# Kernel tuning notes

Hardware: AMD Instinct MI355X
Metric: run time of the kernel (lower is better)

The kernel has to match this reference:

```python
import jax, jax.numpy as jnp
import numpy as np

EPS = 1e-5
HEADS, KK, UU, VV, MM = 4, 16, 1, 64, 23
PAD = (MM - 1) // 2


def _bn(x, gamma, beta, mean, var):
    # eval-mode BatchNorm2d over channel axis 1 of (b, c, w, h)
    scale = gamma / jnp.sqrt(var + EPS)
    return (x - mean[:, None, None]) * scale[:, None, None] + beta[:, None, None]


def setup_inputs() -> dict:
    key = jax.random.key(0)
    ks = jax.random.split(key, 13)
    B, C, W, H = 8, 256, 64, 64
    return {
        "x": jax.random.normal(ks[0], (B, C, W, H), jnp.float32),
        "Wq": jax.random.normal(ks[1], (KK * HEADS, C), jnp.float32) * 0.05,
        "q_gamma": jax.random.uniform(ks[2], (KK * HEADS,), jnp.float32),
        "q_beta": jax.random.normal(ks[3], (KK * HEADS,), jnp.float32) * 0.05,
        "q_mean": jax.random.normal(ks[4], (KK * HEADS,), jnp.float32) * 0.05,
        "q_var": jax.random.uniform(ks[5], (KK * HEADS,), jnp.float32) + 0.5,
        "Wk": jax.random.normal(ks[6], (KK * UU, C), jnp.float32) * 0.05,
        "Wv": jax.random.normal(ks[7], (VV * UU, C), jnp.float32) * 0.05,
        "v_gamma": jax.random.uniform(ks[8], (VV * UU,), jnp.float32),
        "v_beta": jax.random.normal(ks[9], (VV * UU,), jnp.float32) * 0.05,
        "v_mean": jax.random.normal(ks[10], (VV * UU,), jnp.float32) * 0.05,
        "v_var": jax.random.uniform(ks[11], (VV * UU,), jnp.float32) + 0.5,
        "embedding": jax.random.normal(ks[12], (KK, UU, 1, MM, MM), jnp.float32),
    }


def reference(x, Wq, q_gamma, q_beta, q_mean, q_var, Wk, Wv, v_gamma, v_beta, v_mean, v_var, embedding):
    b, C, w, h = x.shape
    n = w * h
    # 1x1 conv projections as channel GEMMs
    q = jnp.einsum('bcij,oc->boij', x, Wq)
    q = _bn(q, q_gamma, q_beta, q_mean, q_var).reshape(b, HEADS, KK, n)
    kf = jnp.einsum('bcij,oc->boij', x, Wk).reshape(b, KK, UU, n)
    kf = jax.nn.softmax(kf, axis=-1)  # softmax over spatial positions
    v = jnp.einsum('bcij,oc->boij', x, Wv)
    v = _bn(v, v_gamma, v_beta, v_mean, v_var)  # (b, vv*uu, w, h)
    v_flat = v.reshape(b, VV, UU, n)
    # content lambda
    lambda_c = jnp.einsum('bkum,bvum->bkv', kf, v_flat)
    y_c = jnp.einsum('bhkn,bkv->bhvn', q, lambda_c)
    # positional lambda via depth-1 conv3d over (vv, w, h)
    v5 = v.reshape(b, UU, VV, w, h)
    lambda_p = jax.lax.conv_general_dilated(
        v5, embedding, window_strides=(1, 1, 1),
        padding=[(0, 0), (PAD, PAD), (PAD, PAD)],
        dimension_numbers=('NCDHW', 'OIDHW', 'NCDHW'))  # (b, kk, vv, w, h)
    lambda_p = lambda_p.reshape(b, KK, VV, n)
    y_p = jnp.einsum('bhkn,bkvn->bhvn', q, lambda_p)
    out = (y_c + y_p).reshape(b, HEADS * VV, w, h)
    return out
```

## Files before the change

kernel.cpp:

```cpp
#include <hip/hip_runtime.h>

typedef __attribute__((ext_vector_type(8))) short bf16x8;
typedef __attribute__((ext_vector_type(4))) float f32x4;

#define EPS 1e-5f
#define B 8
#define C 256
#define NPIX 4096
#define NCH 144
#define ROW_V 64
#define ROW_KF 128
#define PAD 11
#define VH_WORDS 3840

#define WP_OFF    0u
#define BIAS_OFF  36864u
#define PROJ_OFF  37120u
#define RMAX_OFF  4755712u
#define LC_OFF    4755968u
#define ET_OFF    4764160u
#define QT_OFF    4811264u
#define OUTT_OFF  6908416u
#define WS_NEED_QT    6908416u
#define WS_NEED_FULL  15297024u

__device__ inline short f2bf(float f) {
  unsigned u = __float_as_uint(f);
  return (short)((u + 0x7fffu + ((u >> 16) & 1u)) >> 16);
}

__global__ __launch_bounds__(256) void k_prep(
    const float* __restrict__ Wq, const float* __restrict__ qg, const float* __restrict__ qb,
    const float* __restrict__ qm, const float* __restrict__ qv,
    const float* __restrict__ Wk, const float* __restrict__ Wv,
    const float* __restrict__ vg, const float* __restrict__ vb,
    const float* __restrict__ vm, const float* __restrict__ vvar,
    const float* __restrict__ emb,
    float* __restrict__ Wt, float* __restrict__ biasp, ushort* __restrict__ etw) {
  int t = threadIdx.x;
  if (blockIdx.x < 144) {
    int o = blockIdx.x;
    const float* src; float s, bias;
    if (o < 64) {
      s = qg[o] * rsqrtf(qv[o] + EPS); bias = qb[o] - qm[o] * s; src = Wq + o * C;
    } else if (o < 128) {
      int i = o - 64;
      s = vg[i] * rsqrtf(vvar[i] + EPS); bias = vb[i] - vm[i] * s; src = Wv + i * C;
    } else {
      int i = o - 128; s = 1.f; bias = 0.f; src = Wk + i * C;
    }
    Wt[t * NCH + o] = src[t] * s;
    if (t == 0) biasp[o] = bias;
  } else {
    int i = (blockIdx.x - 144) * 256 + t;
    int s = i / 11776;
    int r = i % 11776;
    int dy = r / 512;
    int l = (r / 8) % 64;
    int jj = r % 8;
    int f = l & 15, q = l >> 4;
    int dx = q * 8 + jj - s;
    float val = (dx >= 0 && dx < 23) ? emb[f * 529 + dy * 23 + dx] : 0.f;
    unsigned u = __float_as_uint(val);
    etw[i] = (ushort)((u + 0x7fffu + ((u >> 16) & 1u)) >> 16);
  }
}

__global__ __launch_bounds__(256) void k_wprep(
    const float* __restrict__ Wt, ushort* __restrict__ wtA) {
  int i = blockIdx.x * 256 + threadIdx.x;
  int mt = i >> 9;
  int rest = i & 511;
  int kt = rest >> 6;
  int lane = rest & 63;
  int m = mt * 16 + (lane & 15);
  int c0 = kt * 32 + (lane >> 4) * 8;
  ushort* dst = wtA + (size_t)i * 8;
  #pragma unroll
  for (int j = 0; j < 8; j++) {
    float v = Wt[(c0 + j) * NCH + m];
    unsigned u = __float_as_uint(v);
    dst[j] = (ushort)((u + 0x7fffu + ((u >> 16) & 1u)) >> 16);
  }
}

__global__ __launch_bounds__(256) void k_projm(
    const float* __restrict__ x, const ushort* __restrict__ wtA,
    const float* __restrict__ biasp, float* __restrict__ proj) {
  int ntile = blockIdx.x;
  int b = blockIdx.y;
  int t = threadIdx.x;
  int lane = t & 63, w = t >> 6;
  int px = ntile * 64 + w * 16 + (lane & 15);
  int kq = lane >> 4;
  const float* xb = x + (size_t)b * C * NPIX + px;
  const bf16x8* A = (const bf16x8*)wtA;
  f32x4 acc[9];
  #pragma unroll
  for (int i = 0; i < 9; i++) acc[i] = (f32x4)(0.f);
  #pragma unroll 2
  for (int kt = 0; kt < 8; kt++) {
    int c0 = kt * 32 + kq * 8;
    bf16x8 bb;
    #pragma unroll
    for (int j = 0; j < 8; j++) bb[j] = f2bf(xb[(size_t)(c0 + j) * NPIX]);
    #pragma unroll
    for (int mt = 0; mt < 9; mt++) {
      bf16x8 a = A[(mt * 8 + kt) * 64 + lane];
      acc[mt] = __builtin_amdgcn_mfma_f32_16x16x32_bf16(a, bb, acc[mt], 0, 0, 0);
    }
  }
  float* pb = proj + (size_t)b * NCH * NPIX + px;
  #pragma unroll
  for (int mt = 0; mt < 9; mt++) {
    #pragma unroll
    for (int r = 0; r < 4; r++) {
      int ch = mt * 16 + kq * 4 + r;
      pb[(size_t)ch * NPIX] = acc[mt][r] + biasp[ch];
    }
  }
}

__global__ __launch_bounds__(256) void k_proj(
    const float* __restrict__ x, const float* __restrict__ Wt,
    const float* __restrict__ biasp, float* __restrict__ proj) {
  int tile = blockIdx.x;
  int g = blockIdx.y;
  int b = blockIdx.z;
  int t = threadIdx.x;
  int px = tile * 256 + t;
  const float* xb = x + (size_t)b * C * NPIX + px;
  float acc[18];
  #pragma unroll
  for (int i = 0; i < 18; i++) acc[i] = 0.f;
  #pragma unroll 4
  for (int c = 0; c < C; c++) {
    float xv = xb[(size_t)c * NPIX];
    const float* wrow = Wt + c * NCH + g * 18;
    #pragma unroll
    for (int i = 0; i < 18; i++) acc[i] += xv * wrow[i];
  }
  float* ob = proj + ((size_t)b * NCH + g * 18) * NPIX + px;
  #pragma unroll
  for (int i = 0; i < 18; i++) ob[(size_t)i * NPIX] = acc[i] + biasp[g * 18 + i];
}

__global__ __launch_bounds__(256) void k_qtrans(
    const float* __restrict__ proj, float* __restrict__ qT) {
  int ch = blockIdx.x, b = blockIdx.y, t = threadIdx.x;
  __shared__ float buf[4608];
  const float* src = proj + ((size_t)b * NCH + ch) * NPIX;
  for (int it = 0; it < 16; it++) {
    int p = it * 256 + t;
    buf[p + (p >> 3)] = src[p];
  }
  __syncthreads();
  float* dst = qT + ((size_t)b * 64 + ch) * NPIX;
  for (int it = 0; it < 16; it++) {
    int idx = it * 256 + t;
    int s = idx >> 9, i = idx & 511;
    int p = (i >> 3) * 64 + (i & 7) * 8 + s;
    dst[idx] = buf[p + (p >> 3)];
  }
}

__global__ __launch_bounds__(256) void k_vhalo(
    const float* __restrict__ proj, uint* __restrict__ vhg) {
  int v = blockIdx.x, b = blockIdx.y, t = threadIdx.x;
  const float* vrow = proj + ((size_t)b * NCH + ROW_V + v) * NPIX;
  uint* dst = vhg + (size_t)b * NCH * NPIX + (size_t)v * VH_WORDS;
  for (int p2 = t; p2 < 3784; p2 += 256) {
    int hr = p2 / 44;
    int hc = (p2 % 44) * 2;
    int ir = hr - 11;
    int ic0 = hc - 11, ic1 = hc - 10;
    bool rok = (ir >= 0 && ir < 64);
    float f0 = (rok && ic0 >= 0 && ic0 < 64) ? vrow[ir * 64 + ic0] : 0.f;
    float f1 = (rok && ic1 >= 0 && ic1 < 64) ? vrow[ir * 64 + ic1] : 0.f;
    uint u0 = __float_as_uint(f0), u1 = __float_as_uint(f1);
    uint h0 = (u0 + 0x7fffu + ((u0 >> 16) & 1u)) >> 16;
    uint h1 = (u1 + 0x7fffu + ((u1 >> 16) & 1u)) >> 16;
    dst[p2] = (h0 & 0xffffu) | (h1 << 16);
  }
}

__global__ __launch_bounds__(256) void k_lambda_c(
    const float* __restrict__ proj, float* __restrict__ lc, float* __restrict__ S) {
  int split = blockIdx.x;
  int b = blockIdx.y;
  int t = threadIdx.x;
  int lane = t & 63, w = t >> 6;
  int kr = lane & 15;
  int half = lane >> 4;
  const float* kfrow = proj + ((size_t)b * NCH + ROW_KF + kr) * NPIX;
  const float* vrow  = proj + ((size_t)b * NCH + ROW_V + w * 16 + kr) * NPIX;
  f32x4 acc = (f32x4)(0.f);
  float ssum = 0.f;
  #pragma unroll
  for (int c = 0; c < 2; c++) {
    int n0 = split * 64 + c * 32 + half * 8;
    float4 fa0 = *(const float4*)(kfrow + n0);
    float4 fa1 = *(const float4*)(kfrow + n0 + 4);
    float4 fb0 = *(const float4*)(vrow + n0);
    float4 fb1 = *(const float4*)(vrow + n0 + 4);
    float e0 = __expf(fa0.x), e1 = __expf(fa0.y), e2 = __expf(fa0.z), e3 = __expf(fa0.w);
    float e4 = __expf(fa1.x), e5 = __expf(fa1.y), e6 = __expf(fa1.z), e7 = __expf(fa1.w);
    ssum += (e0 + e1 + e2 + e3) + (e4 + e5 + e6 + e7);
    bf16x8 a, bb;
    a[0] = f2bf(e0); a[1] = f2bf(e1); a[2] = f2bf(e2); a[3] = f2bf(e3);
    a[4] = f2bf(e4); a[5] = f2bf(e5); a[6] = f2bf(e6); a[7] = f2bf(e7);
    bb[0] = f2bf(fb0.x); bb[1] = f2bf(fb0.y); bb[2] = f2bf(fb0.z); bb[3] = f2bf(fb0.w);
    bb[4] = f2bf(fb1.x); bb[5] = f2bf(fb1.y); bb[6] = f2bf(fb1.z); bb[7] = f2bf(fb1.w);
    acc = __builtin_amdgcn_mfma_f32_16x16x32_bf16(a, bb, acc, 0, 0, 0);
  }
  #pragma unroll
  for (int r = 0; r < 4; r++) {
    int k = half * 4 + r;
    atomicAdd(&lc[((size_t)b * 16 + k) * 64 + w * 16 + kr], acc[r]);
  }
  if (w == 0) {
    ssum += __shfl_xor(ssum, 16);
    ssum += __shfl_xor(ssum, 32);
    if (lane < 16) atomicAdd(&S[b * 16 + kr], ssum);
  }
}

__global__ __launch_bounds__(256) void k_lcnorm(
    float* __restrict__ lc, const float* __restrict__ S) {
  int i = blockIdx.x * 256 + threadIdx.x;
  lc[i] /= S[i >> 6];
}

__global__ __launch_bounds__(256, 2) void k_conv_mfma(
    const float* __restrict__ proj, const ushort* __restrict__ etw,
    const float* __restrict__ qT, const float* __restrict__ lc,
    const uint* __restrict__ vhg,
    float* __restrict__ outT, float* __restrict__ out, int mode) {
  int s = blockIdx.x;
  int v = blockIdx.y;
  int b = blockIdx.z;
  int t = threadIdx.x;
  __shared__ __align__(16) ushort vh[86 * 88];

  if (mode != 0) {
    const uint4* vsrc = (const uint4*)(vhg + (size_t)b * NCH * NPIX + (size_t)v * VH_WORDS);
    uint4* vdst = (uint4*)vh;
    for (int i = t; i < 946; i += 256) vdst[i] = vsrc[i];
  } else {
    const float* vrow = proj + ((size_t)b * NCH + ROW_V + v) * NPIX;
    for (int i = t; i < 86 * 88; i += 256) {
      int hr = i / 88, hc = i % 88;
      int ir = hr - 11, ic = hc - 11;
      float val = (ir >= 0 && ir < 64 && ic >= 0 && ic < 64) ? vrow[ir * 64 + ic] : 0.f;
      unsigned u = __float_as_uint(val);
      vh[i] = (ushort)((u + 0x7fffu + ((u >> 16) & 1u)) >> 16);
    }
  }
  __syncthreads();

  int lane = t & 63, w = t >> 6;
  int n_ = lane & 15, q = lane >> 4;
  int rn = n_ >> 3, g = n_ & 7;

  f32x4 acc[8];
  #pragma unroll
  for (int i = 0; i < 8; i++) acc[i] = (f32x4)(0.f);

  const bf16x8* vh8 = (const bf16x8*)vh;
  const bf16x8* e8 = (const bf16x8*)etw + (size_t)s * 1472;
  int baseA = (w * 16 + rn) * 11 + g + q;

  bf16x8 bfr[16];
  #pragma unroll
  for (int r = 0; r < 16; r++)
    bfr[(r & 1) * 8 + ((r >> 1) & 7)] = vh8[baseA + r * 11];

  #pragma unroll
  for (int dy = 0; dy < 23; dy++) {
    bf16x8 ef = e8[dy * 64 + lane];
    bf16x8 tmp;
    if (dy + 16 <= 36) tmp = vh8[baseA + (dy + 16) * 11];
    #pragma unroll
    for (int tt = 0; tt < 8; tt++) {
      int r = dy + 2 * tt;
      acc[tt] = __builtin_amdgcn_mfma_f32_16x16x32_bf16(
          ef, bfr[(r & 1) * 8 + ((r >> 1) & 7)], acc[tt], 0, 0, 0);
    }
    if (dy + 16 <= 36) {
      int rr = dy + 16;
      bfr[(rr & 1) * 8 + ((rr >> 1) & 7)] = tmp;
    }
  }

  float lcv[4];
  #pragma unroll
  for (int r = 0; r < 4; r++) lcv[r] = lc[((size_t)b * 16 + q * 4 + r) * 64 + v];

  if (mode != 0) {
    const float* qTb = qT + (size_t)b * 64 * NPIX;
    float* obT = outT + (size_t)b * 256 * NPIX;
    float* ob = out + (size_t)b * 256 * NPIX;
    #pragma unroll
    for (int tt = 0; tt < 8; tt++) {
      int row = w * 16 + 2 * tt + rn;
      int io = s * 512 + row * 8 + g;
      float lam[4];
      #pragma unroll
      for (int r = 0; r < 4; r++) lam[r] = acc[tt][r] + lcv[r];
      float y[4];
      #pragma unroll
      for (int h = 0; h < 4; h++) {
        float a = 0.f;
        #pragma unroll
        for (int r = 0; r < 4; r++)
          a += qTb[(size_t)(h * 16 + q * 4 + r) * NPIX + io] * lam[r];
        y[h] = a;
      }
      #pragma unroll
      for (int h = 0; h < 4; h++) {
        y[h] += __shfl_xor(y[h], 16);
        y[h] += __shfl_xor(y[h], 32);
      }
      if (q == 0) {
        if (mode == 2) {
          #pragma unroll
          for (int h = 0; h < 4; h++) obT[(size_t)(h * 64 + v) * NPIX + io] = y[h];
        } else {
          int p = row * 64 + 8 * g + s;
          #pragma unroll
          for (int h = 0; h < 4; h++) ob[(size_t)(h * 64 + v) * NPIX + p] = y[h];
        }
      }
    }
  } else {
    const float* qbp = proj + (size_t)b * NCH * NPIX;
    float* ob = out + (size_t)b * 256 * NPIX;
    #pragma unroll
    for (int tt = 0; tt < 8; tt++) {
      int p = (w * 16 + 2 * tt + rn) * 64 + 8 * g + s;
      float lam[4];
      #pragma unroll
      for (int r = 0; r < 4; r++) lam[r] = acc[tt][r] + lcv[r];
      float y[4];
      #pragma unroll
      for (int h = 0; h < 4; h++) {
        float a = 0.f;
        #pragma unroll
        for (int r = 0; r < 4; r++)
          a += qbp[(size_t)(h * 16 + q * 4 + r) * NPIX + p] * lam[r];
        y[h] = a;
      }
      #pragma unroll
      for (int h = 0; h < 4; h++) {
        y[h] += __shfl_xor(y[h], 16);
        y[h] += __shfl_xor(y[h], 32);
      }
      if (q == 0) {
        #pragma unroll
        for (int h = 0; h < 4; h++) ob[(size_t)(h * 64 + v) * NPIX + p] = y[h];
      }
    }
  }
}

__global__ __launch_bounds__(256) void k_outtrans(
    const float* __restrict__ outT, float* __restrict__ out) {
  int ch = blockIdx.x, b = blockIdx.y, t = threadIdx.x;
  __shared__ float buf[4608];
  const float* src = outT + ((size_t)b * 256 + ch) * NPIX;
  for (int it = 0; it < 16; it++) {
    int idx = it * 256 + t;
    int s = idx >> 9, i = idx & 511;
    int p = (i >> 3) * 64 + (i & 7) * 8 + s;
    buf[p + (p >> 3)] = src[idx];
  }
  __syncthreads();
  float* dst = out + ((size_t)b * 256 + ch) * NPIX;
  for (int it = 0; it < 16; it++) {
    int p = it * 256 + t;
    dst[p] = buf[p + (p >> 3)];
  }
}

extern "C" void kernel_launch(void* const* d_in, const int* in_sizes, int n_in,
                              void* d_out, int out_size, void* d_ws, size_t ws_size,
                              hipStream_t stream) {
  const float* x    = (const float*)d_in[0];
  const float* Wq   = (const float*)d_in[1];
  const float* qg   = (const float*)d_in[2];
  const float* qbta = (const float*)d_in[3];
  const float* qm   = (const float*)d_in[4];
  const float* qv   = (const float*)d_in[5];
  const float* Wk   = (const float*)d_in[6];
  const float* Wv   = (const float*)d_in[7];
  const float* vg   = (const float*)d_in[8];
  const float* vb   = (const float*)d_in[9];
  const float* vm   = (const float*)d_in[10];
  const float* vvar = (const float*)d_in[11];
  const float* emb  = (const float*)d_in[12];
  float* ws   = (float*)d_ws;
  float* Wt   = ws + WP_OFF;
  float* bp   = ws + BIAS_OFF;
  float* proj = ws + PROJ_OFF;
  float* Sw   = ws + RMAX_OFF;
  float* lcw  = ws + LC_OFF;
  ushort* etw = (ushort*)(ws + ET_OFF);
  float* qT   = ws + QT_OFF;
  float* outT = ws + OUTT_OFF;
  float* out  = (float*)d_out;
  uint* vhg   = (uint*)proj;
  ushort* wtA = (ushort*)qT;

  size_t wsf = ws_size / sizeof(float);
  int mode = (wsf >= WS_NEED_FULL) ? 2 : ((wsf >= WS_NEED_QT) ? 1 : 0);

  hipLaunchKernelGGL(k_prep, dim3(512), dim3(256), 0, stream,
                     Wq, qg, qbta, qm, qv, Wk, Wv, vg, vb, vm, vvar, emb, Wt, bp, etw);
  hipMemsetAsync(Sw, 0, 8448 * sizeof(float), stream);
  if (mode >= 1) {
    hipLaunchKernelGGL(k_wprep, dim3(18), dim3(256), 0, stream, Wt, wtA);
    hipLaunchKernelGGL(k_projm, dim3(64, 8), dim3(256), 0, stream, x, wtA, bp, proj);
    hipLaunchKernelGGL(k_qtrans, dim3(64, 8), dim3(256), 0, stream, proj, qT);
    hipLaunchKernelGGL(k_vhalo, dim3(64, 8), dim3(256), 0, stream, proj, vhg);
  } else {
    hipLaunchKernelGGL(k_proj, dim3(16, 8, 8), dim3(256), 0, stream, x, Wt, bp, proj);
  }
  hipLaunchKernelGGL(k_lambda_c, dim3(64, 8), dim3(256), 0, stream, proj, lcw, Sw);
  hipLaunchKernelGGL(k_lcnorm, dim3(32), dim3(256), 0, stream, lcw, Sw);
  hipLaunchKernelGGL(k_conv_mfma, dim3(8, 64, 8), dim3(256), 0, stream,
                     proj, etw, qT, lcw, vhg, outT, out, mode);
  if (mode == 2)
    hipLaunchKernelGGL(k_outtrans, dim3(256, 8), dim3(256), 0, stream, outT, out);
}
```

Measured before the change: 212.2 us.

## Fuse q transpose and v halo packing into projection epilogue

The projection MFMA kernel now writes the q channels directly in the transposed qT layout and the v channels directly as bf16 into the padded halo buffer, removing the separate k_qtrans and k_vhalo kernels. The weight bf16 packing (k_wprep) and the zeroing of the halo buffer are folded into extra blocks of k_prep, with wtA staged in the output buffer. This cuts launches and a full read and write pass over the q and v planes, at the cost of scattered 2-byte and strided stores and a larger prep grid that zero-fills the halo.

```diff
diff --git a/kernel.cpp b/kernel.cpp
--- a/kernel.cpp
+++ b/kernel.cpp
@@ -36,10 +36,12 @@
     const float* __restrict__ vg, const float* __restrict__ vb,
     const float* __restrict__ vm, const float* __restrict__ vvar,
     const float* __restrict__ emb,
-    float* __restrict__ Wt, float* __restrict__ biasp, ushort* __restrict__ etw) {
+    float* __restrict__ Wt, float* __restrict__ biasp, ushort* __restrict__ etw,
+    ushort* __restrict__ wtA, uint* __restrict__ vhg) {
   int t = threadIdx.x;
-  if (blockIdx.x < 144) {
-    int o = blockIdx.x;
+  int blk = blockIdx.x;
+  if (blk < 144) {
+    int o = blk;
     const float* src; float s, bias;
     if (o < 64) {
       s = qg[o] * rsqrtf(qv[o] + EPS); bias = qb[o] - qm[o] * s; src = Wq + o * C;
@@ -51,8 +53,8 @@
     }
     Wt[t * NCH + o] = src[t] * s;
     if (t == 0) biasp[o] = bias;
-  } else {
-    int i = (blockIdx.x - 144) * 256 + t;
+  } else if (blk < 512) {
+    int i = (blk - 144) * 256 + t;
     int s = i / 11776;
     int r = i % 11776;
     int dy = r / 512;
@@ -61,37 +63,40 @@
     int f = l & 15, q = l >> 4;
     int dx = q * 8 + jj - s;
     float val = (dx >= 0 && dx < 23) ? emb[f * 529 + dy * 23 + dx] : 0.f;
-    unsigned u = __float_as_uint(val);
-    etw[i] = (ushort)((u + 0x7fffu + ((u >> 16) & 1u)) >> 16);
-  }
-}
-
-__global__ __launch_bounds__(256) void k_wprep(
-    const float* __restrict__ Wt, ushort* __restrict__ wtA) {
-  int i = blockIdx.x * 256 + threadIdx.x;
-  int mt = i >> 9;
-  int rest = i & 511;
-  int kt = rest >> 6;
-  int lane = rest & 63;
-  int m = mt * 16 + (lane & 15);
-  int c0 = kt * 32 + (lane >> 4) * 8;
-  ushort* dst = wtA + (size_t)i * 8;
-  #pragma unroll
-  for (int j = 0; j < 8; j++) {
-    float v = Wt[(c0 + j) * NCH + m];
-    unsigned u = __float_as_uint(v);
-    dst[j] = (ushort)((u + 0x7fffu + ((u >> 16) & 1u)) >> 16);
+    etw[i] = (ushort)f2bf(val);
+  } else if (blk < 530) {
+    int i = (blk - 512) * 256 + t;
+    int mt = i >> 9;
+    int rest = i & 511;
+    int kt = rest >> 6;
+    int lane = rest & 63;
+    int m = mt * 16 + (lane & 15);
+    int c0 = kt * 32 + (lane >> 4) * 8;
+    const float* src; float s;
+    if (m < 64) { s = qg[m] * rsqrtf(qv[m] + EPS); src = Wq + m * C; }
+    else if (m < 128) { int ii = m - 64; s = vg[ii] * rsqrtf(vvar[ii] + EPS); src = Wv + ii * C; }
+    else { s = 1.f; src = Wk + (m - 128) * C; }
+    ushort* dst = wtA + (size_t)i * 8;
+    #pragma unroll
+    for (int j = 0; j < 8; j++) dst[j] = (ushort)f2bf(src[c0 + j] * s);
+  } else {
+    int zi = (blk - 530) * 256 + t;
+    int bb = zi / 61440, w4 = zi % 61440;
+    uint4 z; z.x = z.y = z.z = z.w = 0u;
+    ((uint4*)vhg)[(size_t)bb * 147456 + w4] = z;
   }
 }
 
 __global__ __launch_bounds__(256) void k_projm(
     const float* __restrict__ x, const ushort* __restrict__ wtA,
-    const float* __restrict__ biasp, float* __restrict__ proj) {
+    const float* __restrict__ biasp, float* __restrict__ proj,
+    float* __restrict__ qT, uint* __restrict__ vhg) {
   int ntile = blockIdx.x;
   int b = blockIdx.y;
   int t = threadIdx.x;
   int lane = t & 63, w = t >> 6;
-  int px = ntile * 64 + w * 16 + (lane & 15);
+  int col = w * 16 + (lane & 15);
+  int px = ntile * 64 + col;
   int kq = lane >> 4;
   const float* xb = x + (size_t)b * C * NPIX + px;
   const bf16x8* A = (const bf16x8*)wtA;
@@ -110,13 +115,34 @@
       acc[mt] = __builtin_amdgcn_mfma_f32_16x16x32_bf16(a, bb, acc[mt], 0, 0, 0);
     }
   }
+  int idxT = (col & 7) * 512 + ntile * 8 + (col >> 3);
+  float* qTb = qT + (size_t)b * 64 * NPIX;
+  #pragma unroll
+  for (int mt = 0; mt < 4; mt++) {
+    #pragma unroll
+    for (int r = 0; r < 4; r++) {
+      int ch = mt * 16 + kq * 4 + r;
+      qTb[(size_t)ch * NPIX + idxT] = acc[mt][r] + biasp[ch];
+    }
+  }
   float* pb = proj + (size_t)b * NCH * NPIX + px;
   #pragma unroll
-  for (int mt = 0; mt < 9; mt++) {
+  for (int mt = 4; mt < 9; mt++) {
     #pragma unroll
     for (int r = 0; r < 4; r++) {
       int ch = mt * 16 + kq * 4 + r;
       pb[(size_t)ch * NPIX] = acc[mt][r] + biasp[ch];
+    }
+  }
+  ushort* hb = (ushort*)vhg;
+  size_t hbase = (size_t)b * NCH * NPIX * 2 + (size_t)(ntile + 11) * 88 + col + 11;
+  #pragma unroll
+  for (int mt = 4; mt < 8; mt++) {
+    #pragma unroll
+    for (int r = 0; r < 4; r++) {
+      int ch = mt * 16 + kq * 4 + r;
+      int v = ch - 64;
+      hb[hbase + (size_t)v * (VH_WORDS * 2)] = (ushort)f2bf(acc[mt][r] + biasp[ch]);
     }
   }
 }
@@ -143,45 +169,6 @@
   float* ob = proj + ((size_t)b * NCH + g * 18) * NPIX + px;
   #pragma unroll
   for (int i = 0; i < 18; i++) ob[(size_t)i * NPIX] = acc[i] + biasp[g * 18 + i];
-}
-
-__global__ __launch_bounds__(256) void k_qtrans(
-    const float* __restrict__ proj, float* __restrict__ qT) {
-  int ch = blockIdx.x, b = blockIdx.y, t = threadIdx.x;
-  __shared__ float buf[4608];
-  const float* src = proj + ((size_t)b * NCH + ch) * NPIX;
-  for (int it = 0; it < 16; it++) {
-    int p = it * 256 + t;
-    buf[p + (p >> 3)] = src[p];
-  }
-  __syncthreads();
-  float* dst = qT + ((size_t)b * 64 + ch) * NPIX;
-  for (int it = 0; it < 16; it++) {
-    int idx = it * 256 + t;
-    int s = idx >> 9, i = idx & 511;
-    int p = (i >> 3) * 64 + (i & 7) * 8 + s;
-    dst[idx] = buf[p + (p >> 3)];
-  }
-}
-
-__global__ __launch_bounds__(256) void k_vhalo(
-    const float* __restrict__ proj, uint* __restrict__ vhg) {
-  int v = blockIdx.x, b = blockIdx.y, t = threadIdx.x;
-  const float* vrow = proj + ((size_t)b * NCH + ROW_V + v) * NPIX;
-  uint* dst = vhg + (size_t)b * NCH * NPIX + (size_t)v * VH_WORDS;
-  for (int p2 = t; p2 < 3784; p2 += 256) {
-    int hr = p2 / 44;
-    int hc = (p2 % 44) * 2;
-    int ir = hr - 11;
-    int ic0 = hc - 11, ic1 = hc - 10;
-    bool rok = (ir >= 0 && ir < 64);
-    float f0 = (rok && ic0 >= 0 && ic0 < 64) ? vrow[ir * 64 + ic0] : 0.f;
-    float f1 = (rok && ic1 >= 0 && ic1 < 64) ? vrow[ir * 64 + ic1] : 0.f;
-    uint u0 = __float_as_uint(f0), u1 = __float_as_uint(f1);
-    uint h0 = (u0 + 0x7fffu + ((u0 >> 16) & 1u)) >> 16;
-    uint h1 = (u1 + 0x7fffu + ((u1 >> 16) & 1u)) >> 16;
-    dst[p2] = (h0 & 0xffffu) | (h1 << 16);
-  }
 }
 
 __global__ __launch_bounds__(256) void k_lambda_c(
@@ -409,19 +396,18 @@
   float* outT = ws + OUTT_OFF;
   float* out  = (float*)d_out;
   uint* vhg   = (uint*)proj;
-  ushort* wtA = (ushort*)qT;
+  ushort* wtA = (ushort*)out;
 
   size_t wsf = ws_size / sizeof(float);
   int mode = (wsf >= WS_NEED_FULL) ? 2 : ((wsf >= WS_NEED_QT) ? 1 : 0);
 
-  hipLaunchKernelGGL(k_prep, dim3(512), dim3(256), 0, stream,
-                     Wq, qg, qbta, qm, qv, Wk, Wv, vg, vb, vm, vvar, emb, Wt, bp, etw);
+  hipLaunchKernelGGL(k_prep, dim3(mode >= 1 ? 2450 : 512), dim3(256), 0, stream,
+                     Wq, qg, qbta, qm, qv, Wk, Wv, vg, vb, vm, vvar, emb,
+                     Wt, bp, etw, wtA, vhg);
   hipMemsetAsync(Sw, 0, 8448 * sizeof(float), stream);
   if (mode >= 1) {
-    hipLaunchKernelGGL(k_wprep, dim3(18), dim3(256), 0, stream, Wt, wtA);
-    hipLaunchKernelGGL(k_projm, dim3(64, 8), dim3(256), 0, stream, x, wtA, bp, proj);
-    hipLaunchKernelGGL(k_qtrans, dim3(64, 8), dim3(256), 0, stream, proj, qT);
-    hipLaunchKernelGGL(k_vhalo, dim3(64, 8), dim3(256), 0, stream, proj, vhg);
+    hipLaunchKernelGGL(k_projm, dim3(64, 8), dim3(256), 0, stream,
+                       x, wtA, bp, proj, qT, vhg);
   } else {
     hipLaunchKernelGGL(k_proj, dim3(16, 8, 8), dim3(256), 0, stream, x, Wt, bp, proj);
   }
```

After: 204.8 us. 3.5% less time.
